# Optimization experiments

Measured on AMD Instinct MI355X. Metric: run time of the kernel, lower is better.

Reference implementation:

```python
import jax, jax.numpy as jnp
import numpy as np

EPS = 1e-08


def _similarity_transform(S1, S2):
    """Batched Procrustes: S1, S2 are [B, 3, N]. Returns aligned S1_hat [B, 3, N]."""
    mu1 = jnp.mean(S1, axis=-1, keepdims=True)          # [B,3,1]
    mu2 = jnp.mean(S2, axis=-1, keepdims=True)
    X1 = S1 - mu1
    X2 = S2 - mu2
    var1 = jnp.sum(X1 * X1, axis=(1, 2))                # [B]
    # cross-covariance K = X1 @ X2^T + eps (eps added to every entry, as in torch ref)
    K = jnp.einsum('bin,bjn->bij', X1, X2) + EPS        # [B,3,3]
    U, s, Vh = jnp.linalg.svd(K, full_matrices=False)
    V = jnp.swapaxes(Vh, -1, -2)
    # det(U @ V^T) = det(U @ Vh); sign has zero gradient, same as torch
    sign = jax.lax.stop_gradient(jnp.sign(jnp.linalg.det(jnp.matmul(U, Vh))))  # [B]
    ones = jnp.ones_like(sign)
    d = jnp.stack([ones, ones, sign], axis=-1)          # diag of Z, [B,3]
    # R = V @ Z @ U^T
    R = jnp.einsum('bik,bk,bjk->bij', V, d, U)          # [B,3,3]
    scale = jnp.einsum('bij,bji->b', R, K) / var1       # trace(R@K)/var1, [B]
    t = mu2 - scale[:, None, None] * jnp.matmul(R, mu1)  # [B,3,1]
    S1_hat = scale[:, None, None] * jnp.matmul(R, S1) + t
    return S1_hat


def setup_inputs() -> dict:
    key = jax.random.key(0)
    k1, k2 = jax.random.split(key)
    B, N = 1024, 6890
    pred = jax.random.normal(k1, (B, N, 3), dtype=jnp.float32)
    gt = jax.random.normal(k2, (B, N, 3), dtype=jnp.float32)
    return {"pred": pred, "gt": gt}


def reference(pred, gt):
    # inputs are [B, N, 3] -> torch code transposes to [B, 3, N] and back
    S1 = jnp.swapaxes(pred, 1, 2)
    S2 = jnp.swapaxes(gt, 1, 2)
    S1_hat = jnp.swapaxes(_similarity_transform(S1, S2), 1, 2)  # [B,N,3]
    # loss_type == 'l1', reduction='none'
    return jnp.abs(S1_hat - gt)
```

## Files before the change

### kernel.cpp

```cpp
#include <hip/hip_runtime.h>
#include <math.h>

#define NPTS 6890
#define BATCH 1024
#define FLOATS_PER_BATCH (NPTS * 3)
#define NGROUPS 1722
#define TOTAL_F4 (NGROUPS * 3)
#define TILE_F4 768
#define NTILES 7
#define CHUNKS 2

__device__ __forceinline__ void accum(float* acc, float p0, float p1, float p2,
                                      float g0, float g1, float g2) {
  acc[0] += p0;  acc[1] += p1;  acc[2] += p2;
  acc[3] += g0;  acc[4] += g1;  acc[5] += g2;
  acc[6] += p0 * p0 + p1 * p1 + p2 * p2;
  acc[7]  += p0 * g0;  acc[8]  += p0 * g1;  acc[9]  += p0 * g2;
  acc[10] += p1 * g0;  acc[11] += p1 * g1;  acc[12] += p1 * g2;
  acc[13] += p2 * g0;  acc[14] += p2 * g1;  acc[15] += p2 * g2;
}

__device__ __forceinline__ void accum_group(float* acc,
                                            const float4& a0, const float4& a1,
                                            const float4& a2, const float4& e0,
                                            const float4& e1, const float4& e2) {
  accum(acc, a0.x, a0.y, a0.z, e0.x, e0.y, e0.z);
  accum(acc, a0.w, a1.x, a1.y, e0.w, e1.x, e1.y);
  accum(acc, a1.z, a1.w, a2.x, e1.z, e1.w, e2.x);
  accum(acc, a2.y, a2.z, a2.w, e2.y, e2.z, e2.w);
}

__global__ __launch_bounds__(256, 4) void reduce_kernel(
    const float* __restrict__ pred, const float* __restrict__ gt,
    float* __restrict__ partial) {
  const int b = blockIdx.x;
  const int c = blockIdx.y;
  const size_t ofs0 = (size_t)b * FLOATS_PER_BATCH;
  const int skip = (b & 1) ? 2 : 0;
  const size_t ofs = ofs0 + (size_t)skip * 3;
  const float4* __restrict__ P = (const float4*)(pred + ofs);
  const float4* __restrict__ G = (const float4*)(gt + ofs);

  __shared__ float4 LP[TILE_F4];
  __shared__ float4 LG[TILE_F4];
  __shared__ float red[4][16][17];

  float acc[16];
#pragma unroll
  for (int i = 0; i < 16; ++i) acc[i] = 0.f;

  const int t = (int)threadIdx.x;
  const int tile_beg = (c == 0) ? 0 : 4;
  const int tile_end = (c == 0) ? 4 : NTILES;

  for (int tile = tile_beg; tile < tile_end; ++tile) {
    const int base = tile * TILE_F4;
    const int nf4 = (base + TILE_F4 <= TOTAL_F4) ? TILE_F4 : (TOTAL_F4 - base);
#pragma unroll
    for (int k = 0; k < 3; ++k) {
      const int idx = t + 256 * k;
      if (idx < nf4) {
        LP[idx] = P[base + idx];
        LG[idx] = G[base + idx];
      }
    }
    __syncthreads();
    const int ngr = nf4 / 3;
    if (t < ngr) {
      const float4 a0 = LP[3 * t], a1 = LP[3 * t + 1], a2 = LP[3 * t + 2];
      const float4 e0 = LG[3 * t], e1 = LG[3 * t + 1], e2 = LG[3 * t + 2];
      accum_group(acc, a0, a1, a2, e0, e1, e2);
    }
    __syncthreads();
  }

  if (c == 0 && t < 2) {
    const int n = skip ? t : (NPTS - 2 + t);
    const float* pp = pred + ofs0 + 3 * n;
    const float* gg = gt + ofs0 + 3 * n;
    accum(acc, pp[0], pp[1], pp[2], gg[0], gg[1], gg[2]);
  }

#pragma unroll
  for (int i = 0; i < 16; ++i) {
    acc[i] += __shfl_xor(acc[i], 16, 64);
    acc[i] += __shfl_xor(acc[i], 32, 64);
  }
  const int wave = t >> 6;
  const int lane = t & 63;
  if (lane < 16) {
#pragma unroll
    for (int i = 0; i < 16; ++i) red[wave][lane][i] = acc[i];
  }
  __syncthreads();
  if (t < 16) {
    float s = 0.f;
#pragma unroll
    for (int w = 0; w < 4; ++w)
#pragma unroll
      for (int r = 0; r < 16; ++r) s += red[w][r][t];
    partial[(b * CHUNKS + c) * 16 + t] = s;
  }
}

__global__ void solve_kernel(const float* __restrict__ partial,
                             float* __restrict__ params) {
  const int b = blockIdx.x * blockDim.x + threadIdx.x;
  if (b >= BATCH) return;
  const float* ps = partial + b * (CHUNKS * 16);
  double s[16];
#pragma unroll
  for (int i = 0; i < 16; ++i)
    s[i] = (double)ps[i] + (double)ps[16 + i];

  const double Ninv = 1.0 / (double)NPTS;

  double sp[3] = {s[0], s[1], s[2]};
  double sg[3] = {s[3], s[4], s[5]};
  double mu1[3], mu2[3];
#pragma unroll
  for (int i = 0; i < 3; ++i) { mu1[i] = sp[i] * Ninv; mu2[i] = sg[i] * Ninv; }
  const double var1 =
      s[6] - (sp[0] * sp[0] + sp[1] * sp[1] + sp[2] * sp[2]) * Ninv;

  double K[3][3];
#pragma unroll
  for (int i = 0; i < 3; ++i)
#pragma unroll
    for (int j = 0; j < 3; ++j)
      K[i][j] = s[7 + 3 * i + j] - sp[i] * sg[j] * Ninv + 1e-8;

  double A[3][3];
#pragma unroll
  for (int i = 0; i < 3; ++i)
#pragma unroll
    for (int j = 0; j < 3; ++j)
      A[i][j] = K[0][i] * K[0][j] + K[1][i] * K[1][j] + K[2][i] * K[2][j];

  double V[3][3] = {{1, 0, 0}, {0, 1, 0}, {0, 0, 1}};
  for (int sweep = 0; sweep < 30; ++sweep) {
    const double off = A[0][1] * A[0][1] + A[0][2] * A[0][2] + A[1][2] * A[1][2];
    const double nrm = A[0][0] + A[1][1] + A[2][2];
    if (off <= 1e-30 * nrm * nrm) break;
    for (int pq = 0; pq < 3; ++pq) {
      const int p = (pq == 2) ? 1 : 0;
      const int q = (pq == 0) ? 1 : 2;
      const double apq = A[p][q];
      if (apq == 0.0) continue;
      const double theta = (A[q][q] - A[p][p]) / (2.0 * apq);
      const double tt =
          ((theta >= 0.0) ? 1.0 : -1.0) / (fabs(theta) + sqrt(theta * theta + 1.0));
      const double cc = 1.0 / sqrt(tt * tt + 1.0);
      const double sn = tt * cc;
      const double app = A[p][p], aqq = A[q][q];
      A[p][p] = app - tt * apq;
      A[q][q] = aqq + tt * apq;
      A[p][q] = 0.0; A[q][p] = 0.0;
      const int r = 3 - p - q;
      const double arp = A[r][p], arq = A[r][q];
      A[r][p] = cc * arp - sn * arq; A[p][r] = A[r][p];
      A[r][q] = sn * arp + cc * arq; A[q][r] = A[r][q];
#pragma unroll
      for (int k = 0; k < 3; ++k) {
        const double vkp = V[k][p], vkq = V[k][q];
        V[k][p] = cc * vkp - sn * vkq;
        V[k][q] = sn * vkp + cc * vkq;
      }
    }
  }

  double w[3] = {A[0][0], A[1][1], A[2][2]};
  int i0 = 0, i1 = 1, i2 = 2, tmp;
  if (w[i0] < w[i1]) { tmp = i0; i0 = i1; i1 = tmp; }
  if (w[i0] < w[i2]) { tmp = i0; i0 = i2; i2 = tmp; }
  if (w[i1] < w[i2]) { tmp = i1; i1 = i2; i2 = tmp; }
  const double sv0 = sqrt(fmax(w[i0], 0.0));
  const double sv1 = sqrt(fmax(w[i1], 0.0));
  const double sv2 = sqrt(fmax(w[i2], 0.0));

  const double detK =
      K[0][0] * (K[1][1] * K[2][2] - K[1][2] * K[2][1]) -
      K[0][1] * (K[1][0] * K[2][2] - K[1][2] * K[2][0]) +
      K[0][2] * (K[1][0] * K[2][1] - K[1][1] * K[2][0]);
  const double sgn = (detK > 0.0) ? 1.0 : ((detK < 0.0) ? -1.0 : 0.0);

  const double floor0 = sv0 * 1e-12 + 1e-300;
  const double z0 = 1.0 / fmax(sv0, floor0);
  const double z1 = 1.0 / fmax(sv1, floor0);
  const double z2 = sgn / fmax(sv2, floor0);

  double W[3][3];
#pragma unroll
  for (int a = 0; a < 3; ++a)
#pragma unroll
    for (int c = 0; c < 3; ++c)
      W[a][c] = V[a][i0] * V[c][i0] * z0 + V[a][i1] * V[c][i1] * z1 +
                V[a][i2] * V[c][i2] * z2;

  double R[3][3];
#pragma unroll
  for (int a = 0; a < 3; ++a)
#pragma unroll
    for (int c = 0; c < 3; ++c)
      R[a][c] = W[a][0] * K[c][0] + W[a][1] * K[c][1] + W[a][2] * K[c][2];

  const double trace = sv0 + sv1 + sgn * sv2;
  const double scale = trace / var1;

  float* pr = params + b * 12;
#pragma unroll
  for (int a = 0; a < 3; ++a) {
#pragma unroll
    for (int c = 0; c < 3; ++c) pr[3 * a + c] = (float)(scale * R[a][c]);
    pr[9 + a] = (float)(mu2[a] - scale * (R[a][0] * mu1[0] + R[a][1] * mu1[1] +
                                          R[a][2] * mu1[2]));
  }
}

__device__ __forceinline__ void xform(const float* m, float p0, float p1,
                                      float p2, float g0, float g1, float g2,
                                      float& o0, float& o1, float& o2) {
  o0 = fabsf(m[0] * p0 + m[1] * p1 + m[2] * p2 + m[9] - g0);
  o1 = fabsf(m[3] * p0 + m[4] * p1 + m[5] * p2 + m[10] - g1);
  o2 = fabsf(m[6] * p0 + m[7] * p1 + m[8] * p2 + m[11] - g2);
}

__global__ __launch_bounds__(256) void apply_kernel(
    const float* __restrict__ pred, const float* __restrict__ gt,
    const float* __restrict__ params, float* __restrict__ out) {
  const int b = blockIdx.y;
  const int tile = blockIdx.x;
  float m[12];
#pragma unroll
  for (int i = 0; i < 12; ++i) m[i] = params[b * 12 + i];

  const size_t ofs0 = (size_t)b * FLOATS_PER_BATCH;
  const int skip = (b & 1) ? 2 : 0;
  const size_t ofs = ofs0 + (size_t)skip * 3;
  const float4* __restrict__ P = (const float4*)(pred + ofs);
  const float4* __restrict__ G = (const float4*)(gt + ofs);
  float4* __restrict__ O = (float4*)(out + ofs);

  __shared__ float4 LP[TILE_F4];
  __shared__ float4 LG[TILE_F4];

  const int t = (int)threadIdx.x;
  const int base = tile * TILE_F4;
  const int nf4 = (base + TILE_F4 <= TOTAL_F4) ? TILE_F4 : (TOTAL_F4 - base);

#pragma unroll
  for (int k = 0; k < 3; ++k) {
    const int idx = t + 256 * k;
    if (idx < nf4) {
      LP[idx] = P[base + idx];
      LG[idx] = G[base + idx];
    }
  }
  __syncthreads();

  const int ngr = nf4 / 3;
  if (t < ngr) {
    const float4 a0 = LP[3 * t], a1 = LP[3 * t + 1], a2 = LP[3 * t + 2];
    const float4 c0 = LG[3 * t], c1 = LG[3 * t + 1], c2 = LG[3 * t + 2];
    float4 r0, r1, r2;
    xform(m, a0.x, a0.y, a0.z, c0.x, c0.y, c0.z, r0.x, r0.y, r0.z);
    xform(m, a0.w, a1.x, a1.y, c0.w, c1.x, c1.y, r0.w, r1.x, r1.y);
    xform(m, a1.z, a1.w, a2.x, c1.z, c1.w, c2.x, r1.z, r1.w, r2.x);
    xform(m, a2.y, a2.z, a2.w, c2.y, c2.z, c2.w, r2.y, r2.z, r2.w);
    LP[3 * t] = r0; LP[3 * t + 1] = r1; LP[3 * t + 2] = r2;
  }
  __syncthreads();

#pragma unroll
  for (int k = 0; k < 3; ++k) {
    const int idx = t + 256 * k;
    if (idx < nf4) O[base + idx] = LP[idx];
  }

  if (tile == 0 && t < 2) {
    const int n = skip ? t : (NPTS - 2 + t);
    const float* pp = pred + ofs0 + 3 * n;
    const float* gg = gt + ofs0 + 3 * n;
    float* oo = out + ofs0 + 3 * n;
    xform(m, pp[0], pp[1], pp[2], gg[0], gg[1], gg[2], oo[0], oo[1], oo[2]);
  }
}

extern "C" void kernel_launch(void* const* d_in, const int* in_sizes, int n_in,
                              void* d_out, int out_size, void* d_ws, size_t ws_size,
                              hipStream_t stream) {
  const float* pred = (const float*)d_in[0];
  const float* gt   = (const float*)d_in[1];
  float* out = (float*)d_out;
  float* partial = (float*)d_ws;
  float* params  = partial + BATCH * CHUNKS * 16;

  hipLaunchKernelGGL(reduce_kernel, dim3(BATCH, CHUNKS), dim3(256), 0, stream,
                     pred, gt, partial);
  hipLaunchKernelGGL(solve_kernel, dim3((BATCH + 63) / 64), dim3(64), 0,
                     stream, partial, params);
  hipLaunchKernelGGL(apply_kernel, dim3(NTILES, BATCH), dim3(256), 0, stream,
                     pred, gt, params, out);
}
```

Baseline: 247.5 us.

## Fuse reduce, solve and apply into one register-resident kernel per batch

Replaces the three kernels (reduction, per-batch SVD solve, apply) with one kernel where each 512-thread block loads a whole batch's points into registers. It reduces the statistics, has one thread solve the 3x3 Procrustes problem, then applies the transform from the same registers. This removes the second global read of pred and gt, the workspace round trip and two launches. In exchange, the whole block waits on a serial double-precision Jacobi solve, register pressure is high, and parallelism is one block per batch.

```diff
diff --git a/kernel.cpp b/kernel.cpp
--- a/kernel.cpp
+++ b/kernel.cpp
@@ -5,10 +5,8 @@
 #define BATCH 1024
 #define FLOATS_PER_BATCH (NPTS * 3)
 #define NGROUPS 1722
-#define TOTAL_F4 (NGROUPS * 3)
-#define TILE_F4 768
-#define NTILES 7
-#define CHUNKS 2
+#define NT 512
+
 
 __device__ __forceinline__ void accum(float* acc, float p0, float p1, float p2,
                                       float g0, float g1, float g2) {
@@ -30,193 +28,6 @@
   accum(acc, a2.y, a2.z, a2.w, e2.y, e2.z, e2.w);
 }
 
-__global__ __launch_bounds__(256, 4) void reduce_kernel(
-    const float* __restrict__ pred, const float* __restrict__ gt,
-    float* __restrict__ partial) {
-  const int b = blockIdx.x;
-  const int c = blockIdx.y;
-  const size_t ofs0 = (size_t)b * FLOATS_PER_BATCH;
-  const int skip = (b & 1) ? 2 : 0;
-  const size_t ofs = ofs0 + (size_t)skip * 3;
-  const float4* __restrict__ P = (const float4*)(pred + ofs);
-  const float4* __restrict__ G = (const float4*)(gt + ofs);
-
-  __shared__ float4 LP[TILE_F4];
-  __shared__ float4 LG[TILE_F4];
-  __shared__ float red[4][16][17];
-
-  float acc[16];
-#pragma unroll
-  for (int i = 0; i < 16; ++i) acc[i] = 0.f;
-
-  const int t = (int)threadIdx.x;
-  const int tile_beg = (c == 0) ? 0 : 4;
-  const int tile_end = (c == 0) ? 4 : NTILES;
-
-  for (int tile = tile_beg; tile < tile_end; ++tile) {
-    const int base = tile * TILE_F4;
-    const int nf4 = (base + TILE_F4 <= TOTAL_F4) ? TILE_F4 : (TOTAL_F4 - base);
-#pragma unroll
-    for (int k = 0; k < 3; ++k) {
-      const int idx = t + 256 * k;
-      if (idx < nf4) {
-        LP[idx] = P[base + idx];
-        LG[idx] = G[base + idx];
-      }
-    }
-    __syncthreads();
-    const int ngr = nf4 / 3;
-    if (t < ngr) {
-      const float4 a0 = LP[3 * t], a1 = LP[3 * t + 1], a2 = LP[3 * t + 2];
-      const float4 e0 = LG[3 * t], e1 = LG[3 * t + 1], e2 = LG[3 * t + 2];
-      accum_group(acc, a0, a1, a2, e0, e1, e2);
-    }
-    __syncthreads();
-  }
-
-  if (c == 0 && t < 2) {
-    const int n = skip ? t : (NPTS - 2 + t);
-    const float* pp = pred + ofs0 + 3 * n;
-    const float* gg = gt + ofs0 + 3 * n;
-    accum(acc, pp[0], pp[1], pp[2], gg[0], gg[1], gg[2]);
-  }
-
-#pragma unroll
-  for (int i = 0; i < 16; ++i) {
-    acc[i] += __shfl_xor(acc[i], 16, 64);
-    acc[i] += __shfl_xor(acc[i], 32, 64);
-  }
-  const int wave = t >> 6;
-  const int lane = t & 63;
-  if (lane < 16) {
-#pragma unroll
-    for (int i = 0; i < 16; ++i) red[wave][lane][i] = acc[i];
-  }
-  __syncthreads();
-  if (t < 16) {
-    float s = 0.f;
-#pragma unroll
-    for (int w = 0; w < 4; ++w)
-#pragma unroll
-      for (int r = 0; r < 16; ++r) s += red[w][r][t];
-    partial[(b * CHUNKS + c) * 16 + t] = s;
-  }
-}
-
-__global__ void solve_kernel(const float* __restrict__ partial,
-                             float* __restrict__ params) {
-  const int b = blockIdx.x * blockDim.x + threadIdx.x;
-  if (b >= BATCH) return;
-  const float* ps = partial + b * (CHUNKS * 16);
-  double s[16];
-#pragma unroll
-  for (int i = 0; i < 16; ++i)
-    s[i] = (double)ps[i] + (double)ps[16 + i];
-
-  const double Ninv = 1.0 / (double)NPTS;
-
-  double sp[3] = {s[0], s[1], s[2]};
-  double sg[3] = {s[3], s[4], s[5]};
-  double mu1[3], mu2[3];
-#pragma unroll
-  for (int i = 0; i < 3; ++i) { mu1[i] = sp[i] * Ninv; mu2[i] = sg[i] * Ninv; }
-  const double var1 =
-      s[6] - (sp[0] * sp[0] + sp[1] * sp[1] + sp[2] * sp[2]) * Ninv;
-
-  double K[3][3];
-#pragma unroll
-  for (int i = 0; i < 3; ++i)
-#pragma unroll
-    for (int j = 0; j < 3; ++j)
-      K[i][j] = s[7 + 3 * i + j] - sp[i] * sg[j] * Ninv + 1e-8;
-
-  double A[3][3];
-#pragma unroll
-  for (int i = 0; i < 3; ++i)
-#pragma unroll
-    for (int j = 0; j < 3; ++j)
-      A[i][j] = K[0][i] * K[0][j] + K[1][i] * K[1][j] + K[2][i] * K[2][j];
-
-  double V[3][3] = {{1, 0, 0}, {0, 1, 0}, {0, 0, 1}};
-  for (int sweep = 0; sweep < 30; ++sweep) {
-    const double off = A[0][1] * A[0][1] + A[0][2] * A[0][2] + A[1][2] * A[1][2];
-    const double nrm = A[0][0] + A[1][1] + A[2][2];
-    if (off <= 1e-30 * nrm * nrm) break;
-    for (int pq = 0; pq < 3; ++pq) {
-      const int p = (pq == 2) ? 1 : 0;
-      const int q = (pq == 0) ? 1 : 2;
-      const double apq = A[p][q];
-      if (apq == 0.0) continue;
-      const double theta = (A[q][q] - A[p][p]) / (2.0 * apq);
-      const double tt =
-          ((theta >= 0.0) ? 1.0 : -1.0) / (fabs(theta) + sqrt(theta * theta + 1.0));
-      const double cc = 1.0 / sqrt(tt * tt + 1.0);
-      const double sn = tt * cc;
-      const double app = A[p][p], aqq = A[q][q];
-      A[p][p] = app - tt * apq;
-      A[q][q] = aqq + tt * apq;
-      A[p][q] = 0.0; A[q][p] = 0.0;
-      const int r = 3 - p - q;
-      const double arp = A[r][p], arq = A[r][q];
-      A[r][p] = cc * arp - sn * arq; A[p][r] = A[r][p];
-      A[r][q] = sn * arp + cc * arq; A[q][r] = A[r][q];
-#pragma unroll
-      for (int k = 0; k < 3; ++k) {
-        const double vkp = V[k][p], vkq = V[k][q];
-        V[k][p] = cc * vkp - sn * vkq;
-        V[k][q] = sn * vkp + cc * vkq;
-      }
-    }
-  }
-
-  double w[3] = {A[0][0], A[1][1], A[2][2]};
-  int i0 = 0, i1 = 1, i2 = 2, tmp;
-  if (w[i0] < w[i1]) { tmp = i0; i0 = i1; i1 = tmp; }
-  if (w[i0] < w[i2]) { tmp = i0; i0 = i2; i2 = tmp; }
-  if (w[i1] < w[i2]) { tmp = i1; i1 = i2; i2 = tmp; }
-  const double sv0 = sqrt(fmax(w[i0], 0.0));
-  const double sv1 = sqrt(fmax(w[i1], 0.0));
-  const double sv2 = sqrt(fmax(w[i2], 0.0));
-
-  const double detK =
-      K[0][0] * (K[1][1] * K[2][2] - K[1][2] * K[2][1]) -
-      K[0][1] * (K[1][0] * K[2][2] - K[1][2] * K[2][0]) +
-      K[0][2] * (K[1][0] * K[2][1] - K[1][1] * K[2][0]);
-  const double sgn = (detK > 0.0) ? 1.0 : ((detK < 0.0) ? -1.0 : 0.0);
-
-  const double floor0 = sv0 * 1e-12 + 1e-300;
-  const double z0 = 1.0 / fmax(sv0, floor0);
-  const double z1 = 1.0 / fmax(sv1, floor0);
-  const double z2 = sgn / fmax(sv2, floor0);
-
-  double W[3][3];
-#pragma unroll
-  for (int a = 0; a < 3; ++a)
-#pragma unroll
-    for (int c = 0; c < 3; ++c)
-      W[a][c] = V[a][i0] * V[c][i0] * z0 + V[a][i1] * V[c][i1] * z1 +
-                V[a][i2] * V[c][i2] * z2;
-
-  double R[3][3];
-#pragma unroll
-  for (int a = 0; a < 3; ++a)
-#pragma unroll
-    for (int c = 0; c < 3; ++c)
-      R[a][c] = W[a][0] * K[c][0] + W[a][1] * K[c][1] + W[a][2] * K[c][2];
-
-  const double trace = sv0 + sv1 + sgn * sv2;
-  const double scale = trace / var1;
-
-  float* pr = params + b * 12;
-#pragma unroll
-  for (int a = 0; a < 3; ++a) {
-#pragma unroll
-    for (int c = 0; c < 3; ++c) pr[3 * a + c] = (float)(scale * R[a][c]);
-    pr[9 + a] = (float)(mu2[a] - scale * (R[a][0] * mu1[0] + R[a][1] * mu1[1] +
-                                          R[a][2] * mu1[2]));
-  }
-}
-
 __device__ __forceinline__ void xform(const float* m, float p0, float p1,
                                       float p2, float g0, float g1, float g2,
                                       float& o0, float& o1, float& o2) {
@@ -225,15 +36,47 @@
   o2 = fabsf(m[6] * p0 + m[7] * p1 + m[8] * p2 + m[11] - g2);
 }
 
-__global__ __launch_bounds__(256) void apply_kernel(
+__device__ __forceinline__ void apply_group(const float* m,
+                                            const float4& a0, const float4& a1,
+                                            const float4& a2, const float4& e0,
+                                            const float4& e1, const float4& e2,
+                                            float4& r0, float4& r1, float4& r2) {
+  xform(m, a0.x, a0.y, a0.z, e0.x, e0.y, e0.z, r0.x, r0.y, r0.z);
+  xform(m, a0.w, a1.x, a1.y, e0.w, e1.x, e1.y, r0.w, r1.x, r1.y);
+  xform(m, a1.z, a1.w, a2.x, e1.z, e1.w, e2.x, r1.z, r1.w, r2.x);
+  xform(m, a2.y, a2.z, a2.w, e2.y, e2.z, e2.w, r2.y, r2.z, r2.w);
+}
+
+#define JROT(p, q, r)                                                         \
+  do {                                                                        \
+    const double apq = A[p][q];                                               \
+    if (apq != 0.0) {                                                         \
+      const double theta = (A[q][q] - A[p][p]) / (2.0 * apq);                 \
+      const double tt = ((theta >= 0.0) ? 1.0 : -1.0) /                       \
+                        (fabs(theta) + sqrt(theta * theta + 1.0));            \
+      const double cc = 1.0 / sqrt(tt * tt + 1.0);                            \
+      const double sn = tt * cc;                                              \
+      const double app = A[p][p], aqq = A[q][q];                              \
+      A[p][p] = app - tt * apq;                                               \
+      A[q][q] = aqq + tt * apq;                                               \
+      A[p][q] = 0.0; A[q][p] = 0.0;                                          \
+      const double arp = A[r][p], arq = A[r][q];                              \
+      A[r][p] = cc * arp - sn * arq; A[p][r] = A[r][p];                       \
+      A[r][q] = sn * arp + cc * arq; A[q][r] = A[r][q];                       \
+      _Pragma("unroll")                                                       \
+      for (int k = 0; k < 3; ++k) {                                           \
+        const double vkp = V[k][p], vkq = V[k][q];                            \
+        V[k][p] = cc * vkp - sn * vkq;                                        \
+        V[k][q] = sn * vkp + cc * vkq;                                        \
+      }                                                                       \
+    }                                                                         \
+  } while (0)
+
+__global__ __launch_bounds__(NT, 2) void fused_kernel(
     const float* __restrict__ pred, const float* __restrict__ gt,
-    const float* __restrict__ params, float* __restrict__ out) {
-  const int b = blockIdx.y;
-  const int tile = blockIdx.x;
-  float m[12];
-#pragma unroll
-  for (int i = 0; i < 12; ++i) m[i] = params[b * 12 + i];
-
+    float* __restrict__ out) {
+  const int b = blockIdx.x;
+  const int t = (int)threadIdx.x;
   const size_t ofs0 = (size_t)b * FLOATS_PER_BATCH;
   const int skip = (b & 1) ? 2 : 0;
   const size_t ofs = ofs0 + (size_t)skip * 3;
@@ -241,48 +84,192 @@
   const float4* __restrict__ G = (const float4*)(gt + ofs);
   float4* __restrict__ O = (float4*)(out + ofs);
 
-  __shared__ float4 LP[TILE_F4];
-  __shared__ float4 LG[TILE_F4];
-
-  const int t = (int)threadIdx.x;
-  const int base = tile * TILE_F4;
-  const int nf4 = (base + TILE_F4 <= TOTAL_F4) ? TILE_F4 : (TOTAL_F4 - base);
-
+  __shared__ float red[8][16][17];
+  __shared__ float sums_lds[16];
+  __shared__ float pm[12];
+
+  float4 rp[4][3], rg[4][3];
+  const bool has3 = (t < NGROUPS - 3 * NT);
 #pragma unroll
   for (int k = 0; k < 3; ++k) {
-    const int idx = t + 256 * k;
-    if (idx < nf4) {
-      LP[idx] = P[base + idx];
-      LG[idx] = G[base + idx];
-    }
-  }
-  __syncthreads();
-
-  const int ngr = nf4 / 3;
-  if (t < ngr) {
-    const float4 a0 = LP[3 * t], a1 = LP[3 * t + 1], a2 = LP[3 * t + 2];
-    const float4 c0 = LG[3 * t], c1 = LG[3 * t + 1], c2 = LG[3 * t + 2];
-    float4 r0, r1, r2;
-    xform(m, a0.x, a0.y, a0.z, c0.x, c0.y, c0.z, r0.x, r0.y, r0.z);
-    xform(m, a0.w, a1.x, a1.y, c0.w, c1.x, c1.y, r0.w, r1.x, r1.y);
-    xform(m, a1.z, a1.w, a2.x, c1.z, c1.w, c2.x, r1.z, r1.w, r2.x);
-    xform(m, a2.y, a2.z, a2.w, c2.y, c2.z, c2.w, r2.y, r2.z, r2.w);
-    LP[3 * t] = r0; LP[3 * t + 1] = r1; LP[3 * t + 2] = r2;
-  }
-  __syncthreads();
-
-#pragma unroll
-  for (int k = 0; k < 3; ++k) {
-    const int idx = t + 256 * k;
-    if (idx < nf4) O[base + idx] = LP[idx];
-  }
-
-  if (tile == 0 && t < 2) {
+    const int g = t + NT * k;
+    rp[k][0] = P[3 * g]; rp[k][1] = P[3 * g + 1]; rp[k][2] = P[3 * g + 2];
+    rg[k][0] = G[3 * g]; rg[k][1] = G[3 * g + 1]; rg[k][2] = G[3 * g + 2];
+  }
+  if (has3) {
+    const int g = t + NT * 3;
+    rp[3][0] = P[3 * g]; rp[3][1] = P[3 * g + 1]; rp[3][2] = P[3 * g + 2];
+    rg[3][0] = G[3 * g]; rg[3][1] = G[3 * g + 1]; rg[3][2] = G[3 * g + 2];
+  }
+  float lp0 = 0.f, lp1 = 0.f, lp2 = 0.f, lg0 = 0.f, lg1 = 0.f, lg2 = 0.f;
+  const bool hasL = (t < 2);
+  if (hasL) {
     const int n = skip ? t : (NPTS - 2 + t);
     const float* pp = pred + ofs0 + 3 * n;
     const float* gg = gt + ofs0 + 3 * n;
+    lp0 = pp[0]; lp1 = pp[1]; lp2 = pp[2];
+    lg0 = gg[0]; lg1 = gg[1]; lg2 = gg[2];
+  }
+
+  float acc[16];
+#pragma unroll
+  for (int i = 0; i < 16; ++i) acc[i] = 0.f;
+#pragma unroll
+  for (int k = 0; k < 3; ++k)
+    accum_group(acc, rp[k][0], rp[k][1], rp[k][2], rg[k][0], rg[k][1], rg[k][2]);
+  if (has3)
+    accum_group(acc, rp[3][0], rp[3][1], rp[3][2], rg[3][0], rg[3][1], rg[3][2]);
+  if (hasL) accum(acc, lp0, lp1, lp2, lg0, lg1, lg2);
+
+#pragma unroll
+  for (int i = 0; i < 16; ++i) {
+    acc[i] += __shfl_xor(acc[i], 16, 64);
+    acc[i] += __shfl_xor(acc[i], 32, 64);
+  }
+  const int wave = t >> 6;
+  const int lane = t & 63;
+  if (lane < 16) {
+#pragma unroll
+    for (int i = 0; i < 16; ++i) red[wave][lane][i] = acc[i];
+  }
+  __syncthreads();
+  if (t < 16) {
+    float s = 0.f;
+#pragma unroll
+    for (int w = 0; w < 8; ++w)
+#pragma unroll
+      for (int r = 0; r < 16; ++r) s += red[w][r][t];
+    sums_lds[t] = s;
+  }
+  __syncthreads();
+
+  if (t == 0) {
+    double s[16];
+#pragma unroll
+    for (int i = 0; i < 16; ++i) s[i] = (double)sums_lds[i];
+    const double Ninv = 1.0 / (double)NPTS;
+    double sp[3] = {s[0], s[1], s[2]};
+    double sg[3] = {s[3], s[4], s[5]};
+    double mu1[3], mu2[3];
+#pragma unroll
+    for (int i = 0; i < 3; ++i) { mu1[i] = sp[i] * Ninv; mu2[i] = sg[i] * Ninv; }
+    const double var1 =
+        s[6] - (sp[0] * sp[0] + sp[1] * sp[1] + sp[2] * sp[2]) * Ninv;
+
+    double K[3][3];
+#pragma unroll
+    for (int i = 0; i < 3; ++i)
+#pragma unroll
+      for (int j = 0; j < 3; ++j)
+        K[i][j] = s[7 + 3 * i + j] - sp[i] * sg[j] * Ninv + 1e-8;
+
+    double A[3][3];
+#pragma unroll
+    for (int i = 0; i < 3; ++i)
+#pragma unroll
+      for (int j = 0; j < 3; ++j)
+        A[i][j] = K[0][i] * K[0][j] + K[1][i] * K[1][j] + K[2][i] * K[2][j];
+
+    double V[3][3] = {{1, 0, 0}, {0, 1, 0}, {0, 0, 1}};
+    for (int sweep = 0; sweep < 30; ++sweep) {
+      const double off =
+          A[0][1] * A[0][1] + A[0][2] * A[0][2] + A[1][2] * A[1][2];
+      const double nrm = A[0][0] + A[1][1] + A[2][2];
+      if (off <= 1e-30 * nrm * nrm) break;
+      JROT(0, 1, 2);
+      JROT(0, 2, 1);
+      JROT(1, 2, 0);
+    }
+
+    double wv[3] = {A[0][0], A[1][1], A[2][2]};
+    if (wv[0] < wv[1]) {
+      double tw = wv[0]; wv[0] = wv[1]; wv[1] = tw;
+#pragma unroll
+      for (int k = 0; k < 3; ++k) {
+        double tv = V[k][0]; V[k][0] = V[k][1]; V[k][1] = tv;
+      }
+    }
+    if (wv[0] < wv[2]) {
+      double tw = wv[0]; wv[0] = wv[2]; wv[2] = tw;
+#pragma unroll
+      for (int k = 0; k < 3; ++k) {
+        double tv = V[k][0]; V[k][0] = V[k][2]; V[k][2] = tv;
+      }
+    }
+    if (wv[1] < wv[2]) {
+      double tw = wv[1]; wv[1] = wv[2]; wv[2] = tw;
+#pragma unroll
+      for (int k = 0; k < 3; ++k) {
+        double tv = V[k][1]; V[k][1] = V[k][2]; V[k][2] = tv;
+      }
+    }
+    const double sv0 = sqrt(fmax(wv[0], 0.0));
+    const double sv1 = sqrt(fmax(wv[1], 0.0));
+    const double sv2 = sqrt(fmax(wv[2], 0.0));
+
+    const double detK =
+        K[0][0] * (K[1][1] * K[2][2] - K[1][2] * K[2][1]) -
+        K[0][1] * (K[1][0] * K[2][2] - K[1][2] * K[2][0]) +
+        K[0][2] * (K[1][0] * K[2][1] - K[1][1] * K[2][0]);
+    const double sgn = (detK > 0.0) ? 1.0 : ((detK < 0.0) ? -1.0 : 0.0);
+
+    const double floor0 = sv0 * 1e-12 + 1e-300;
+    const double z0 = 1.0 / fmax(sv0, floor0);
+    const double z1 = 1.0 / fmax(sv1, floor0);
+    const double z2 = sgn / fmax(sv2, floor0);
+
+    double W[3][3];
+#pragma unroll
+    for (int a = 0; a < 3; ++a)
+#pragma unroll
+      for (int c = 0; c < 3; ++c)
+        W[a][c] = V[a][0] * V[c][0] * z0 + V[a][1] * V[c][1] * z1 +
+                  V[a][2] * V[c][2] * z2;
+
+    double R[3][3];
+#pragma unroll
+    for (int a = 0; a < 3; ++a)
+#pragma unroll
+      for (int c = 0; c < 3; ++c)
+        R[a][c] = W[a][0] * K[c][0] + W[a][1] * K[c][1] + W[a][2] * K[c][2];
+
+    const double trace = sv0 + sv1 + sgn * sv2;
+    const double scale = trace / var1;
+
+#pragma unroll
+    for (int a = 0; a < 3; ++a) {
+#pragma unroll
+      for (int c = 0; c < 3; ++c) pm[3 * a + c] = (float)(scale * R[a][c]);
+      pm[9 + a] = (float)(mu2[a] - scale * (R[a][0] * mu1[0] +
+                                            R[a][1] * mu1[1] +
+                                            R[a][2] * mu1[2]));
+    }
+  }
+  __syncthreads();
+
+  float m[12];
+#pragma unroll
+  for (int i = 0; i < 12; ++i) m[i] = pm[i];
+
+#pragma unroll
+  for (int k = 0; k < 3; ++k) {
+    const int g = t + NT * k;
+    float4 r0, r1, r2;
+    apply_group(m, rp[k][0], rp[k][1], rp[k][2], rg[k][0], rg[k][1], rg[k][2],
+                r0, r1, r2);
+    O[3 * g] = r0; O[3 * g + 1] = r1; O[3 * g + 2] = r2;
+  }
+  if (has3) {
+    const int g = t + NT * 3;
+    float4 r0, r1, r2;
+    apply_group(m, rp[3][0], rp[3][1], rp[3][2], rg[3][0], rg[3][1], rg[3][2],
+                r0, r1, r2);
+    O[3 * g] = r0; O[3 * g + 1] = r1; O[3 * g + 2] = r2;
+  }
+  if (hasL) {
+    const int n = skip ? t : (NPTS - 2 + t);
     float* oo = out + ofs0 + 3 * n;
-    xform(m, pp[0], pp[1], pp[2], gg[0], gg[1], gg[2], oo[0], oo[1], oo[2]);
+    xform(m, lp0, lp1, lp2, lg0, lg1, lg2, oo[0], oo[1], oo[2]);
   }
 }
 
@@ -292,13 +279,6 @@
   const float* pred = (const float*)d_in[0];
   const float* gt   = (const float*)d_in[1];
   float* out = (float*)d_out;
-  float* partial = (float*)d_ws;
-  float* params  = partial + BATCH * CHUNKS * 16;
-
-  hipLaunchKernelGGL(reduce_kernel, dim3(BATCH, CHUNKS), dim3(256), 0, stream,
-                     pred, gt, partial);
-  hipLaunchKernelGGL(solve_kernel, dim3((BATCH + 63) / 64), dim3(64), 0,
-                     stream, partial, params);
-  hipLaunchKernelGGL(apply_kernel, dim3(NTILES, BATCH), dim3(256), 0, stream,
-                     pred, gt, params, out);
-}
+  hipLaunchKernelGGL(fused_kernel, dim3(BATCH), dim3(NT), 0, stream,
+                     pred, gt, out);
+}
```

After: 235.9 us. 1.05x faster.
